# Kernel tuning notes

Measured on AMD Instinct MI355X. Metric: run time of the kernel, lower is better.

Reference implementation:

```python
import jax, jax.numpy as jnp
import numpy as np

EPS = 1e-5
R_MAX = 2.0
KPTS = 4

def silu(x):
    return x * jax.nn.sigmoid(x)

def conv1x1(x, w):  # w: (O, I)
    return jnp.einsum('oi,bihw->bohw', w, x)

def dwconv3(x, k):  # k: (C, 1, 3, 3), depthwise
    return jax.lax.conv_general_dilated(x, k, (1, 1), 'SAME',
        feature_group_count=x.shape[1], dimension_numbers=('NCHW', 'OIHW', 'NCHW'))

def conv3x3(x, k):  # k: (O, I, 3, 3)
    return jax.lax.conv_general_dilated(x, k, (1, 1), 'SAME',
        dimension_numbers=('NCHW', 'OIHW', 'NCHW'))

def bn_eval(x, g, b, m, v):
    scale = g / jnp.sqrt(v + EPS)
    return x * scale[None, :, None, None] + (b - m * scale)[None, :, None, None]

def ds_block(x, dw, pw, g, b, m, v):  # _DS: dwconv3 -> 1x1 -> BN -> SiLU
    return silu(bn_eval(conv1x1(dwconv3(x, dw), pw), g, b, m, v))

def offset_attn_head(q, w1, w2, b2):
    h = silu(conv3x3(q, w1))
    out = conv1x1(h, w2) + b2[None, :, None, None]
    B, _, H, W = out.shape
    off = out[:, :2 * KPTS].reshape(B, KPTS, 2, H, W)
    w = jax.nn.softmax(out[:, 2 * KPTS:].reshape(B, KPTS, H, W), axis=1)
    return off, w

def make_base_grid(Hf, Wf, Hc, Wc):
    yy, xx = jnp.meshgrid(jnp.arange(Hf, dtype=jnp.float32),
                          jnp.arange(Wf, dtype=jnp.float32), indexing='ij')
    xc = (xx + 0.5) * (Wc / Wf) - 0.5
    yc = (yy + 0.5) * (Hc / Hf) - 0.5
    gx = 2.0 * xc / max(Wc - 1, 1) - 1.0
    gy = 2.0 * yc / max(Hc - 1, 1) - 1.0
    return jnp.stack((gx, gy), axis=-1)  # (Hf, Wf, 2)

def avgpool(x, f):  # exact adaptive_avg_pool2d when H,W divisible by f
    B, C, H, W = x.shape
    return x.reshape(B, C, H // f, f, W // f, f).mean(axis=(3, 5))

def _gather(imgf, idx):  # imgf (C, HW), idx (K, Hf, Wf) -> (C, K, Hf, Wf)
    return imgf[:, idx]

def deform_sample(coarse, off, w, base, r_max=R_MAX):
    # bilinear grid_sample, padding_mode='border', align_corners=True
    B, C, Hc, Wc = coarse.shape
    K = off.shape[1]
    step_x = 2.0 / max(Wc - 1, 1)
    step_y = 2.0 / max(Hc - 1, 1)
    gx = base[..., 0][None, None] + jnp.tanh(off[:, :, 0]) * (r_max * step_x)  # (B,K,Hf,Wf)
    gy = base[..., 1][None, None] + jnp.tanh(off[:, :, 1]) * (r_max * step_y)
    ix = jnp.clip((gx + 1.0) * 0.5 * (Wc - 1), 0.0, Wc - 1)  # border padding = clamp
    iy = jnp.clip((gy + 1.0) * 0.5 * (Hc - 1), 0.0, Hc - 1)
    x0 = jnp.floor(ix); y0 = jnp.floor(iy)
    wx = (ix - x0)[:, None]  # (B,1,K,Hf,Wf)
    wy = (iy - y0)[:, None]
    x0i = x0.astype(jnp.int32); y0i = y0.astype(jnp.int32)
    x1i = jnp.minimum(x0i + 1, Wc - 1); y1i = jnp.minimum(y0i + 1, Hc - 1)
    imgf = coarse.reshape(B, C, Hc * Wc)
    g = jax.vmap(_gather)
    v00 = g(imgf, y0i * Wc + x0i)  # (B,C,K,Hf,Wf)
    v01 = g(imgf, y0i * Wc + x1i)
    v10 = g(imgf, y1i * Wc + x0i)
    v11 = g(imgf, y1i * Wc + x1i)
    samp = (v00 * (1 - wx) * (1 - wy) + v01 * wx * (1 - wy)
            + v10 * (1 - wx) * wy + v11 * wx * wy)
    return jnp.einsum('bkhw,bckhw->bchw', w, samp)

def csdm(x, ds0_dw, ds0_pw, ds0_g, ds0_b, ds0_m, ds0_v,
         ds1_dw, ds1_pw, ds1_g, ds1_b, ds1_m, ds1_v,
         ds2_dw, ds2_pw, ds2_g, ds2_b, ds2_m, ds2_v,
         qproj_w, h1_w1, h1_w2, h1_b2, h2_w1, h2_w2, h2_b2,
         r_w1, r_b1, r_w2, r_b2, final_w):
    B, C, H, W = x.shape
    s1 = avgpool(x, 2)
    s2 = avgpool(x, 4)
    z0 = ds_block(x,  ds0_dw, ds0_pw, ds0_g, ds0_b, ds0_m, ds0_v)
    z1 = ds_block(s1, ds1_dw, ds1_pw, ds1_g, ds1_b, ds1_m, ds1_v)
    z2 = ds_block(s2, ds2_dw, ds2_pw, ds2_g, ds2_b, ds2_m, ds2_v)
    q = conv1x1(z0, qproj_w)
    off1, w1 = offset_attn_head(q, h1_w1, h1_w2, h1_b2)
    off2, w2 = offset_attn_head(q, h2_w1, h2_w2, h2_b2)
    base1 = make_base_grid(H, W, z1.shape[2], z1.shape[3])
    base2 = make_base_grid(H, W, z2.shape[2], z2.shape[3])
    y1 = deform_sample(z1, off1, w1, base1)
    y2 = deform_sample(z2, off2, w2, base2)
    d0 = z0.mean(axis=(2, 3))
    d1 = y1.mean(axis=(2, 3))
    d2 = y2.mean(axis=(2, 3))
    hid = silu(jnp.concatenate([d0, d1, d2], axis=-1) @ r_w1 + r_b1)
    alpha = jax.nn.softmax(hid @ r_w2 + r_b2, axis=-1)  # (B, 3)
    a = alpha[:, :, None, None, None]
    out = a[:, 0] * z0 + a[:, 1] * y1 + a[:, 2] * y2
    return x + conv1x1(out, final_w)

def setup_inputs() -> dict:
    key = jax.random.key(0)
    B, C, H, W = 4, 32, 256, 256
    h, hr = 16, 32  # head hidden = max(4, int(C*0.5)); router hidden = max(16, C)
    ks = jax.random.split(key, 40)
    n = lambda i, shape, s=0.2: jax.random.normal(ks[i], shape, jnp.float32) * s
    inp = {'x': jax.random.normal(ks[0], (B, C, H, W), jnp.float32)}
    for j, p in enumerate(['ds0', 'ds1', 'ds2']):
        b = 1 + 6 * j
        inp[p + '_dw'] = n(b, (C, 1, 3, 3))
        inp[p + '_pw'] = n(b + 1, (C, C))
        inp[p + '_g'] = jnp.ones((C,), jnp.float32)
        inp[p + '_b'] = jnp.zeros((C,), jnp.float32)
        inp[p + '_m'] = n(b + 4, (C,), 0.1)
        inp[p + '_v'] = 1.0 + jax.random.uniform(ks[b + 5], (C,), jnp.float32) * 0.1
    inp['qproj_w'] = n(20, (C, C))
    inp['h1_w1'] = n(21, (h, C, 3, 3)); inp['h1_w2'] = n(22, (3 * KPTS, h)); inp['h1_b2'] = n(23, (3 * KPTS,), 0.1)
    inp['h2_w1'] = n(24, (h, C, 3, 3)); inp['h2_w2'] = n(25, (3 * KPTS, h)); inp['h2_b2'] = n(26, (3 * KPTS,), 0.1)
    inp['r_w1'] = n(27, (3 * C, hr)); inp['r_b1'] = n(28, (hr,), 0.1)
    inp['r_w2'] = n(29, (hr, 3)); inp['r_b2'] = n(30, (3,), 0.1)
    inp['final_w'] = n(31, (C, C))
    return inp

def reference(x, ds0_dw, ds0_pw, ds0_g, ds0_b, ds0_m, ds0_v,
              ds1_dw, ds1_pw, ds1_g, ds1_b, ds1_m, ds1_v,
              ds2_dw, ds2_pw, ds2_g, ds2_b, ds2_m, ds2_v,
              qproj_w, h1_w1, h1_w2, h1_b2, h2_w1, h2_w2, h2_b2,
              r_w1, r_b1, r_w2, r_b2, final_w):
    return csdm(x, ds0_dw, ds0_pw, ds0_g, ds0_b, ds0_m, ds0_v,
                ds1_dw, ds1_pw, ds1_g, ds1_b, ds1_m, ds1_v,
                ds2_dw, ds2_pw, ds2_g, ds2_b, ds2_m, ds2_v,
                qproj_w, h1_w1, h1_w2, h1_b2, h2_w1, h2_w2, h2_b2,
                r_w1, r_b1, r_w2, r_b2, final_w)
```

## Files before the change

kernel.cpp:

```cpp
#include <hip/hip_runtime.h>
#include <math.h>


constexpr int B = 4, C = 32, H = 256, W = 256;
constexpr int HW = H * W;
constexpr int H1 = 128, W1 = 128, HW1 = H1 * W1;
constexpr int H2 = 64,  W2 = 64,  HW2 = H2 * W2;
constexpr int CH = 16;
constexpr int CO = 12;
constexpr int TILE = 16;
constexpr int HALO = 18;
constexpr int TAREA = HALO * HALO;
constexpr int WP = 258;

typedef unsigned short ushort_t;
typedef __attribute__((ext_vector_type(8))) short bf16x8;
typedef __attribute__((ext_vector_type(4))) float f32x4;
typedef __attribute__((ext_vector_type(2))) float v2f;

static __device__ __forceinline__ float fast_rcp(float x) { return __builtin_amdgcn_rcpf(x); }
static __device__ __forceinline__ float silu_f(float x) { return x * fast_rcp(1.0f + __expf(-x)); }
static __device__ __forceinline__ v2f silu2(v2f x) {
    v2f r; r.x = silu_f(x.x); r.y = silu_f(x.y); return r;
}
static __device__ __forceinline__ float tanh_f(float x) {
    float xc = fminf(fmaxf(x, -15.0f), 15.0f);
    float e = __expf(2.0f * xc);
    return (e - 1.0f) * fast_rcp(e + 1.0f);
}
static __device__ __forceinline__ ushort_t f2b(float f) {
    unsigned u = __float_as_uint(f);
    return (ushort_t)((u + 0x7fffu + ((u >> 16) & 1u)) >> 16);
}
static __device__ __forceinline__ float bl(unsigned u) { return __uint_as_float(u << 16); }
static __device__ __forceinline__ float bh(unsigned u) { return __uint_as_float(u & 0xffff0000u); }
static __device__ __forceinline__ float wave_sum(float s) {
    s += __shfl_xor(s, 32, 64); s += __shfl_xor(s, 16, 64);
    s += __shfl_xor(s, 8, 64);  s += __shfl_xor(s, 4, 64);
    s += __shfl_xor(s, 2, 64);  s += __shfl_xor(s, 1, 64);
    return s;
}

static __device__ __forceinline__ float red8_ch(float v0, float v1, float v2, float v3,
                                                float v4, float v5, float v6, float v7,
                                                int lane) {
    bool q0 = (lane & 1) != 0, q1 = (lane & 2) != 0, q2 = (lane & 4) != 0;
    float a0 = (q0 ? v4 : v0) + __shfl_xor(q0 ? v0 : v4, 1, 64);
    float a1 = (q0 ? v5 : v1) + __shfl_xor(q0 ? v1 : v5, 1, 64);
    float a2 = (q0 ? v6 : v2) + __shfl_xor(q0 ? v2 : v6, 1, 64);
    float a3 = (q0 ? v7 : v3) + __shfl_xor(q0 ? v3 : v7, 1, 64);
    float c0 = (q1 ? a2 : a0) + __shfl_xor(q1 ? a0 : a2, 2, 64);
    float c1 = (q1 ? a3 : a1) + __shfl_xor(q1 ? a1 : a3, 2, 64);
    float e  = (q2 ? c1 : c0) + __shfl_xor(q2 ? c0 : c1, 4, 64);
    e += __shfl_xor(e, 8, 64);
    e += __shfl_xor(e, 16, 64);
    e += __shfl_xor(e, 32, 64);
    return e;
}

__global__ void pre_kernel(const float* __restrict__ x, float* __restrict__ s1,
                           ushort_t* __restrict__ qpad, float* __restrict__ dall,
                           const float* __restrict__ h1w1, const float* __restrict__ h2w1,
                           ushort_t* __restrict__ w1ra, ushort_t* __restrict__ w1rb) {
    int idx = blockIdx.x * blockDim.x + threadIdx.x;
    constexpr int NP = B * C * HW1;
    if (idx < NP) {
        int wo = idx % W1; int t = idx / W1;
        int ho = t % H1;   t /= H1;
        const float* src = x + ((size_t)t * H + (size_t)ho * 2) * W + (size_t)wo * 2;
        s1[idx] = (src[0] + src[1] + src[W] + src[W + 1]) * 0.25f;
        return;
    }
    int i = idx - NP;
    if (i < 4112) {
        int b = i / 1028, r = i % 1028;
        int y, xx;
        if (r < 258)      { y = 0;           xx = r; }
        else if (r < 516) { y = 257;         xx = r - 258; }
        else if (r < 772) { y = r - 516 + 1; xx = 0; }
        else              { y = r - 772 + 1; xx = 257; }
        uint4 z4 = {0, 0, 0, 0};
        uint4* p = (uint4*)(qpad + (((size_t)b * WP + y) * WP + xx) * 32);
        p[0] = z4; p[1] = z4; p[2] = z4; p[3] = z4;
        return;
    }
    i -= 4112;
    if (i < 512) { dall[i] = 0.0f; return; }
    i -= 512;
    if (i < 4608) {
        int o = i / 288, k = i - o * 288;
        int j = k >> 5, ci = k & 31;
        w1ra[i] = f2b(h1w1[(o * C + ci) * 9 + j]);
        return;
    }
    i -= 4608;
    if (i < 4608) {
        int o = i / 288, k = i - o * 288;
        int j = k >> 5, ci = k & 31;
        w1rb[i] = f2b(h2w1[(o * C + ci) * 9 + j]);
    }
}

__global__ void pool4_kernel(const float* __restrict__ s1, float* __restrict__ s2) {
    int idx = blockIdx.x * blockDim.x + threadIdx.x;
    if (idx >= B * C * HW2) return;
    int wo = idx % W2; int t = idx / W2;
    int ho = t % H2;   t /= H2;
    const float* src = s1 + ((size_t)t * H1 + (size_t)ho * 2) * W1 + (size_t)wo * 2;
    s2[idx] = (src[0] + src[1] + src[W1] + src[W1 + 1]) * 0.25f;
}

template<bool CHLAST>
__global__ __launch_bounds__(256, 4) void fused_ds_kernel(
        const float* __restrict__ in, const float* __restrict__ dw,
        const float* __restrict__ pw, const float* __restrict__ g,
        const float* __restrict__ bb, const float* __restrict__ m,
        const float* __restrict__ v, const float* __restrict__ qw,
        float* __restrict__ out, ushort_t* __restrict__ outcl,
        ushort_t* __restrict__ qout, float* __restrict__ dall,
        int Hs, int Ws, int tilesX) {
    __shared__ unsigned tileu[16 * TAREA];
    __shared__ v2f dwp[16 * 9];
    __shared__ v2f pwp[C * 16];
    __shared__ v2f qwp[CHLAST ? 1 : C * 16];
    __shared__ v2f scale2[16], shift2[16];
    __shared__ float zsum[CHLAST ? 1 : 4][CHLAST ? 1 : 32];
    int tid = threadIdx.x;
    int b = blockIdx.y;
    int HWs = Hs * Ws;
    int ox = (blockIdx.x % tilesX) * TILE;
    int oy = (blockIdx.x / tilesX) * TILE;

    for (int i = tid; i < 16 * 9; i += 256) {
        int c2 = i / 9, j = i - c2 * 9;
        dwp[i] = (v2f){dw[(2 * c2) * 9 + j], dw[(2 * c2 + 1) * 9 + j]};
    }
    for (int i = tid; i < C * 16; i += 256) {
        int ci = i >> 4, o2 = i & 15;
        pwp[i] = (v2f){pw[(2 * o2) * C + ci], pw[(2 * o2 + 1) * C + ci]};
        if (!CHLAST) qwp[i] = (v2f){qw[(2 * o2) * C + ci], qw[(2 * o2 + 1) * C + ci]};
    }
    if (tid < 16) {
        float s0 = g[2 * tid] * rsqrtf(v[2 * tid] + 1e-5f);
        float s1v = g[2 * tid + 1] * rsqrtf(v[2 * tid + 1] + 1e-5f);
        scale2[tid] = (v2f){s0, s1v};
        shift2[tid] = (v2f){bb[2 * tid] - m[2 * tid] * s0, bb[2 * tid + 1] - m[2 * tid + 1] * s1v};
    }
    const float* src = in + (size_t)b * C * HWs;
    for (int i = tid; i < 16 * TAREA; i += 256) {
        int c2 = i / TAREA, r = i - c2 * TAREA;
        int yy = r / HALO, xx = r - yy * HALO;
        int gy = oy - 1 + yy, gx = ox - 1 + xx;
        float v0 = 0.0f, v1 = 0.0f;
        if (gy >= 0 && gy < Hs && gx >= 0 && gx < Ws) {
            const float* sp = src + (size_t)(2 * c2) * HWs + gy * Ws + gx;
            v0 = sp[0]; v1 = sp[HWs];
        }
        tileu[i] = (unsigned)f2b(v0) | ((unsigned)f2b(v1) << 16);
    }
    __syncthreads();

    int tx = tid & 15, ty = tid >> 4;
    int off[9];
#pragma unroll
    for (int jy = 0; jy < 3; ++jy)
#pragma unroll
        for (int jx = 0; jx < 3; ++jx)
            off[jy * 3 + jx] = (ty + jy) * HALO + tx + jx;

    v2f t2[16];
#pragma unroll
    for (int c2 = 0; c2 < 16; ++c2) {
        v2f s = {0.0f, 0.0f};
        const unsigned* tp = tileu + c2 * TAREA;
#pragma unroll
        for (int j = 0; j < 9; ++j) {
            unsigned u = tp[off[j]];
            v2f val = {bl(u), bh(u)};
            s += dwp[c2 * 9 + j] * val;
        }
        t2[c2] = s;
    }

    v2f acc2[16];
#pragma unroll
    for (int o2 = 0; o2 < 16; ++o2) acc2[o2] = (v2f){0.0f, 0.0f};
#pragma unroll
    for (int i2 = 0; i2 < 16; ++i2) {
        float ta = t2[i2].x, tb = t2[i2].y;
        const v2f* r0 = pwp + (2 * i2) * 16;
        const v2f* r1 = r0 + 16;
#pragma unroll
        for (int o2 = 0; o2 < 16; ++o2)
            acc2[o2] += r0[o2] * ta + r1[o2] * tb;
    }
#pragma unroll
    for (int o2 = 0; o2 < 16; ++o2)
        acc2[o2] = silu2(acc2[o2] * scale2[o2] + shift2[o2]);

    int px = ox + tx, py = oy + ty;
    int p = py * Ws + px;
    if (CHLAST) {
        unsigned up[16];
#pragma unroll
        for (int j = 0; j < 16; ++j)
            up[j] = (unsigned)f2b(acc2[j].x) | ((unsigned)f2b(acc2[j].y) << 16);
        uint4* dst = (uint4*)(outcl + ((size_t)b * HWs + p) * C);
#pragma unroll
        for (int j = 0; j < 4; ++j)
            dst[j] = make_uint4(up[4 * j], up[4 * j + 1], up[4 * j + 2], up[4 * j + 3]);
    } else {
        float* dst = out + (size_t)b * C * HWs + p;
#pragma unroll
        for (int o2 = 0; o2 < 16; ++o2) {
            dst[(size_t)(2 * o2) * HWs] = acc2[o2].x;
            dst[(size_t)(2 * o2 + 1) * HWs] = acc2[o2].y;
        }
        v2f q2[16];
#pragma unroll
        for (int o2 = 0; o2 < 16; ++o2) q2[o2] = (v2f){0.0f, 0.0f};
#pragma unroll
        for (int i2 = 0; i2 < 16; ++i2) {
            float ta = acc2[i2].x, tb = acc2[i2].y;
            const v2f* r0 = qwp + (2 * i2) * 16;
            const v2f* r1 = r0 + 16;
#pragma unroll
            for (int o2 = 0; o2 < 16; ++o2)
                q2[o2] += r0[o2] * ta + r1[o2] * tb;
        }
        unsigned up[16];
#pragma unroll
        for (int j = 0; j < 16; ++j)
            up[j] = (unsigned)f2b(q2[j].x) | ((unsigned)f2b(q2[j].y) << 16);
        uint4* qd = (uint4*)(qout + (((size_t)b * WP + py + 1) * WP + px + 1) * 32);
#pragma unroll
        for (int j = 0; j < 4; ++j)
            qd[j] = make_uint4(up[4 * j], up[4 * j + 1], up[4 * j + 2], up[4 * j + 3]);
        int lane = tid & 63, wv = tid >> 6;
#pragma unroll
        for (int o2 = 0; o2 < 16; ++o2) {
            float sx = wave_sum(acc2[o2].x);
            float sy = wave_sum(acc2[o2].y);
            if (lane == 0) { zsum[wv][2 * o2] = sx; zsum[wv][2 * o2 + 1] = sy; }
        }
        __syncthreads();
        if (tid < 32)
            atomicAdd(&dall[b * 96 + tid],
                      (zsum[0][tid] + zsum[1][tid] + zsum[2][tid] + zsum[3][tid]) * (1.0f / HW));
    }
}

template<int HC, int WC>
static __device__ __forceinline__ void calc_off(const float* o12, int px, int py,
                                                int* zoff, float* wgt) {
    float mx = fmaxf(fmaxf(o12[8], o12[9]), fmaxf(o12[10], o12[11]));
    float e0 = __expf(o12[8] - mx), e1 = __expf(o12[9] - mx);
    float e2 = __expf(o12[10] - mx), e3 = __expf(o12[11] - mx);
    float inv = fast_rcp(e0 + e1 + e2 + e3);
    float wk4[4] = {e0 * inv, e1 * inv, e2 * inv, e3 * inv};
    float xc = (px + 0.5f) * ((float)WC / (float)W) - 0.5f;
    float yc = (py + 0.5f) * ((float)HC / (float)H) - 0.5f;
#pragma unroll
    for (int k = 0; k < 4; ++k) {
        float ix = fminf(fmaxf(xc + 2.0f * tanh_f(o12[2 * k]),     0.0f), (float)(WC - 1));
        float iy = fminf(fmaxf(yc + 2.0f * tanh_f(o12[2 * k + 1]), 0.0f), (float)(HC - 1));
        float x0f = floorf(ix), y0f = floorf(iy);
        int x0 = (int)x0f, y0 = (int)y0f;
        int x1 = min(x0 + 1, WC - 1), y1 = min(y0 + 1, HC - 1);
        float wx = ix - x0f, wy = iy - y0f;
        float wk = wk4[k];
        zoff[4 * k + 0] = (y0 * WC + x0) * C; wgt[4 * k + 0] = (1.0f - wx) * (1.0f - wy) * wk;
        zoff[4 * k + 1] = (y0 * WC + x1) * C; wgt[4 * k + 1] = wx * (1.0f - wy) * wk;
        zoff[4 * k + 2] = (y1 * WC + x0) * C; wgt[4 * k + 2] = (1.0f - wx) * wy * wk;
        zoff[4 * k + 3] = (y1 * WC + x1) * C; wgt[4 * k + 3] = wx * wy * wk;
    }
}

__global__ __launch_bounds__(256, 4) void head_deform_kernel(
        const ushort_t* __restrict__ qpad,
        const ushort_t* __restrict__ z1, const ushort_t* __restrict__ z2,
        const ushort_t* __restrict__ w1ra, const ushort_t* __restrict__ w1rb,
        const float* __restrict__ w2a, const float* __restrict__ b2a,
        const float* __restrict__ w2b, const float* __restrict__ b2b,
        float* __restrict__ y1, float* __restrict__ y2, float* __restrict__ dall) {
    __shared__ __align__(16) char smem[TAREA * C * 2];
    ushort_t* tile = (ushort_t*)smem;
    unsigned* hidw = (unsigned*)smem;
    float (*ysum)[32] = (float (*)[32])(smem + 9216);
    int tid = threadIdx.x, b = blockIdx.y, hsel = blockIdx.z;
    int ox = (blockIdx.x & 15) * TILE, oy = (blockIdx.x >> 4) * TILE;
    int lane = tid & 63, wv = tid >> 6;
    int n15 = lane & 15, quad = lane >> 4;
    int tx = tid & 15, ty = tid >> 4;

    {
        const ushort_t* base = qpad + ((size_t)b * WP + oy) * WP * 32;
        uint4* tl = (uint4*)tile;
        for (int i = tid; i < 1296; i += 256) {
            int yy = i / 72, r = i - yy * 72;
            tl[i] = *(const uint4*)(base + ((size_t)yy * WP + ox) * 32 + r * 8);
        }
    }
    __syncthreads();

    const ushort_t* w1r = hsel ? w1rb : w1ra;
    bf16x8 af[9];
#pragma unroll
    for (int j = 0; j < 9; ++j)
        af[j] = *(const bf16x8*)(w1r + n15 * 288 + j * 32 + quad * 8);
    unsigned pk[8];
#pragma unroll
    for (int g = 0; g < 4; ++g) {
        int yrow = wv * 4 + g;
        f32x4 acc = {0.0f, 0.0f, 0.0f, 0.0f};
#pragma unroll
        for (int jy = 0; jy < 3; ++jy)
#pragma unroll
            for (int jx = 0; jx < 3; ++jx) {
                const bf16x8* bp = (const bf16x8*)(tile +
                    ((yrow + jy) * HALO + n15 + jx) * 32 + quad * 8);
                acc = __builtin_amdgcn_mfma_f32_16x16x32_bf16(
                    af[jy * 3 + jx], *bp, acc, 0, 0, 0);
            }
        pk[2 * g]     = (unsigned)f2b(acc[0]) | ((unsigned)f2b(acc[1]) << 16);
        pk[2 * g + 1] = (unsigned)f2b(acc[2]) | ((unsigned)f2b(acc[3]) << 16);
    }
    __syncthreads();
#pragma unroll
    for (int g = 0; g < 4; ++g) {
        int pxl = (wv * 4 + g) * 16 + n15;
        hidw[pxl * 9 + quad * 2]     = pk[2 * g];
        hidw[pxl * 9 + quad * 2 + 1] = pk[2 * g + 1];
    }
    float hid[CH];
#pragma unroll
    for (int j = 0; j < 8; ++j) {
        unsigned u = hidw[tid * 9 + j];
        hid[2 * j]     = silu_f(bl(u));
        hid[2 * j + 1] = silu_f(bh(u));
    }

    const float* w2 = hsel ? w2b : w2a;
    const float* bs = hsel ? b2b : b2a;
    float o12[CO];
#pragma unroll
    for (int j = 0; j < CO; ++j) {
        float a = bs[j];
#pragma unroll
        for (int i = 0; i < CH; ++i) a += w2[j * CH + i] * hid[i];
        o12[j] = a;
    }
    int px = ox + tx, py = oy + ty;
    int off[16]; float wg[16];
    if (hsel == 0) calc_off<H1, W1>(o12, px, py, off, wg);
    else           calc_off<H2, W2>(o12, px, py, off, wg);

    const ushort_t* zb = hsel ? z2 + (size_t)b * HW2 * C : z1 + (size_t)b * HW1 * C;
    int p = py * W + px;
    float* d = (hsel ? y2 : y1) + (size_t)b * C * HW + p;

#pragma unroll
    for (int c8 = 0; c8 < 4; ++c8) {
        uint4 vv[16];
#pragma unroll
        for (int j = 0; j < 16; ++j)
            vv[j] = *(const uint4*)(zb + off[j] + c8 * 8);
        f32x4 lo = {0.0f, 0.0f, 0.0f, 0.0f};
        f32x4 hi = {0.0f, 0.0f, 0.0f, 0.0f};
#pragma unroll
        for (int j = 0; j < 16; ++j) {
            float wj = wg[j];
            lo[0] += wj * bl(vv[j].x); lo[1] += wj * bh(vv[j].x);
            lo[2] += wj * bl(vv[j].y); lo[3] += wj * bh(vv[j].y);
            hi[0] += wj * bl(vv[j].z); hi[1] += wj * bh(vv[j].z);
            hi[2] += wj * bl(vv[j].w); hi[3] += wj * bh(vv[j].w);
        }
#pragma unroll
        for (int k = 0; k < 4; ++k) {
            d[(size_t)(c8 * 8 + k) * HW]     = lo[k];
            d[(size_t)(c8 * 8 + 4 + k) * HW] = hi[k];
        }
        float s = red8_ch(lo[0], lo[1], lo[2], lo[3], hi[0], hi[1], hi[2], hi[3], lane);
        if (lane < 8)
            ysum[wv][c8 * 8 + ((lane & 1) * 4 + (lane & 2) + ((lane >> 2) & 1))] = s;
    }
    __syncthreads();
    if (tid < 32) {
        float s = ysum[0][tid] + ysum[1][tid] + ysum[2][tid] + ysum[3][tid];
        atomicAdd(&dall[b * 96 + 32 + hsel * 32 + tid], s * (1.0f / HW));
    }
}

__global__ void gate_kernel(const float* __restrict__ dall,
                            const float* __restrict__ w1, const float* __restrict__ b1,
                            const float* __restrict__ w2, const float* __restrict__ b2,
                            float* __restrict__ alpha) {
    __shared__ float hid[B][32];
    int tid = threadIdx.x;
    int b = tid >> 5, j = tid & 31;
    float a = b1[j];
    for (int k = 0; k < 96; ++k) a += dall[b * 96 + k] * w1[k * 32 + j];
    hid[b][j] = silu_f(a);
    __syncthreads();
    if (j == 0) {
        float lg[3];
#pragma unroll
        for (int t = 0; t < 3; ++t) {
            float acc = b2[t];
            for (int jj = 0; jj < 32; ++jj) acc += hid[b][jj] * w2[jj * 3 + t];
            lg[t] = acc;
        }
        float mx = fmaxf(lg[0], fmaxf(lg[1], lg[2]));
        float e0 = __expf(lg[0] - mx), e1 = __expf(lg[1] - mx), e2 = __expf(lg[2] - mx);
        float inv = fast_rcp(e0 + e1 + e2);
        alpha[b * 3 + 0] = e0 * inv;
        alpha[b * 3 + 1] = e1 * inv;
        alpha[b * 3 + 2] = e2 * inv;
    }
}

__global__ __launch_bounds__(256, 4) void final_kernel(
        const float* __restrict__ x,
        const float* __restrict__ z0, const float* __restrict__ y1,
        const float* __restrict__ y2, const float* __restrict__ alpha,
        const float* __restrict__ fw, float* __restrict__ out) {
    __shared__ float ws[C * C];
    for (int i = threadIdx.x; i < C * C; i += blockDim.x) ws[i] = fw[i];
    __syncthreads();
    int idx = blockIdx.x * blockDim.x + threadIdx.x;
    constexpr int HP = HW / 2;
    if (idx >= B * HP) return;
    int b = idx / HP, p = (idx - b * HP) * 2;
    float a0 = alpha[b * 3], a1 = alpha[b * 3 + 1], a2 = alpha[b * 3 + 2];
    size_t base = (size_t)b * C * HW + p;
    v2f mix[C];
#pragma unroll
    for (int i = 0; i < C; ++i) {
        size_t e = base + (size_t)i * HW;
        v2f za = *(const v2f*)(z0 + e);
        v2f ya = *(const v2f*)(y1 + e);
        v2f yb = *(const v2f*)(y2 + e);
        mix[i] = a0 * za + a1 * ya + a2 * yb;
    }
#pragma unroll 4
    for (int o = 0; o < C; ++o) {
        v2f acc = {0.0f, 0.0f};
#pragma unroll
        for (int i = 0; i < C; ++i) acc += ws[o * C + i] * mix[i];
        size_t e = base + (size_t)o * HW;
        v2f xr = *(const v2f*)(x + e);
        *(v2f*)(out + e) = acc + xr;
    }
}

extern "C" void kernel_launch(void* const* d_in, const int* in_sizes, int n_in,
                              void* d_out, int out_size, void* d_ws, size_t ws_size,
                              hipStream_t stream) {
    const float* x       = (const float*)d_in[0];
    const float* ds_dw[3] = {(const float*)d_in[1],  (const float*)d_in[7],  (const float*)d_in[13]};
    const float* ds_pw[3] = {(const float*)d_in[2],  (const float*)d_in[8],  (const float*)d_in[14]};
    const float* ds_g[3]  = {(const float*)d_in[3],  (const float*)d_in[9],  (const float*)d_in[15]};
    const float* ds_b[3]  = {(const float*)d_in[4],  (const float*)d_in[10], (const float*)d_in[16]};
    const float* ds_m[3]  = {(const float*)d_in[5],  (const float*)d_in[11], (const float*)d_in[17]};
    const float* ds_v[3]  = {(const float*)d_in[6],  (const float*)d_in[12], (const float*)d_in[18]};
    const float* qproj_w = (const float*)d_in[19];
    const float* h1_w1   = (const float*)d_in[20];
    const float* h1_w2   = (const float*)d_in[21];
    const float* h1_b2   = (const float*)d_in[22];
    const float* h2_w1   = (const float*)d_in[23];
    const float* h2_w2   = (const float*)d_in[24];
    const float* h2_b2   = (const float*)d_in[25];
    const float* r_w1    = (const float*)d_in[26];
    const float* r_b1    = (const float*)d_in[27];
    const float* r_w2    = (const float*)d_in[28];
    const float* r_b2    = (const float*)d_in[29];
    const float* final_w = (const float*)d_in[30];
    float* out = (float*)d_out;

    constexpr size_t N0 = (size_t)B * C * HW;
    constexpr size_t N1 = (size_t)B * C * HW1;
    constexpr size_t N2 = (size_t)B * C * HW2;
    constexpr size_t NQ = ((size_t)B * WP * WP * 32 + 1) / 2;

    float* w = (float*)d_ws;
    float* z0   = w; w += N0;
    float* y1   = w; w += N0;
    float* y2   = w; w += N0;
    ushort_t* z1cl = (ushort_t*)w; w += N1 / 2;
    ushort_t* z2cl = (ushort_t*)w; w += N2 / 2;
    float* s1   = w; w += N1;
    float* s2   = w; w += N2;
    ushort_t* qpad = (ushort_t*)w; w += NQ;
    ushort_t* w1ra = (ushort_t*)w; w += 2304;
    ushort_t* w1rb = (ushort_t*)w; w += 2304;
    float* dall  = w; w += 512;
    float* alpha = w; w += 16;
    (void)ws_size; (void)in_sizes; (void)n_in; (void)out_size;

    const int T = 256;
    auto g = [](size_t n, int t) { return (int)((n + t - 1) / t); };

    pre_kernel<<<g(N1 + 4112 + 512 + 9216, T), T, 0, stream>>>(
        x, s1, qpad, dall, h1_w1, h2_w1, w1ra, w1rb);
    pool4_kernel<<<g(N2, T), T, 0, stream>>>(s1, s2);

    fused_ds_kernel<false><<<dim3((H / TILE) * (W / TILE), B), T, 0, stream>>>(
        x, ds_dw[0], ds_pw[0], ds_g[0], ds_b[0], ds_m[0], ds_v[0], qproj_w,
        z0, nullptr, qpad, dall, H, W, W / TILE);
    fused_ds_kernel<true><<<dim3((H1 / TILE) * (W1 / TILE), B), T, 0, stream>>>(
        s1, ds_dw[1], ds_pw[1], ds_g[1], ds_b[1], ds_m[1], ds_v[1], nullptr,
        nullptr, z1cl, nullptr, nullptr, H1, W1, W1 / TILE);
    fused_ds_kernel<true><<<dim3((H2 / TILE) * (W2 / TILE), B), T, 0, stream>>>(
        s2, ds_dw[2], ds_pw[2], ds_g[2], ds_b[2], ds_m[2], ds_v[2], nullptr,
        nullptr, z2cl, nullptr, nullptr, H2, W2, W2 / TILE);

    head_deform_kernel<<<dim3((H / TILE) * (W / TILE), B, 2), T, 0, stream>>>(
        qpad, z1cl, z2cl, w1ra, w1rb, h1_w2, h1_b2, h2_w2, h2_b2, y1, y2, dall);

    gate_kernel<<<1, 128, 0, stream>>>(dall, r_w1, r_b1, r_w2, r_b2, alpha);

    final_kernel<<<g((size_t)B * HW / 2, T), T, 0, stream>>>(x, z0, y1, y2, alpha, final_w, out);
}
```

Baseline: 327.3 us.

## Merge pyramid pooling and three DS levels into fewer launches

Computes the 4x4 pooled input directly from x inside pre_kernel, which removes the separate pool4 launch and its dependency on s1. The three per-level depthwise-separable kernel launches are merged into one grid whose blocks pick their level from blockIdx, so the small coarse levels run concurrently with the fine level instead of serializing. The channel-sum reduction also switches from 32 full wave_sum butterflies to the packed red8_ch reduction, cutting shuffle count. In exchange the merged kernel loses template specialization, adding runtime branches and possibly more register pressure for the coarse-level blocks.

```diff
diff --git a/kernel.cpp b/kernel.cpp
--- a/kernel.cpp
+++ b/kernel.cpp
@@ -34,12 +34,6 @@
 }
 static __device__ __forceinline__ float bl(unsigned u) { return __uint_as_float(u << 16); }
 static __device__ __forceinline__ float bh(unsigned u) { return __uint_as_float(u & 0xffff0000u); }
-static __device__ __forceinline__ float wave_sum(float s) {
-    s += __shfl_xor(s, 32, 64); s += __shfl_xor(s, 16, 64);
-    s += __shfl_xor(s, 8, 64);  s += __shfl_xor(s, 4, 64);
-    s += __shfl_xor(s, 2, 64);  s += __shfl_xor(s, 1, 64);
-    return s;
-}
 
 static __device__ __forceinline__ float red8_ch(float v0, float v1, float v2, float v3,
                                                 float v4, float v5, float v6, float v7,
@@ -59,11 +53,13 @@
 }
 
 __global__ void pre_kernel(const float* __restrict__ x, float* __restrict__ s1,
+                           float* __restrict__ s2,
                            ushort_t* __restrict__ qpad, float* __restrict__ dall,
                            const float* __restrict__ h1w1, const float* __restrict__ h2w1,
                            ushort_t* __restrict__ w1ra, ushort_t* __restrict__ w1rb) {
     int idx = blockIdx.x * blockDim.x + threadIdx.x;
     constexpr int NP = B * C * HW1;
+    constexpr int NP2 = B * C * HW2;
     if (idx < NP) {
         int wo = idx % W1; int t = idx / W1;
         int ho = t % H1;   t /= H1;
@@ -72,6 +68,20 @@
         return;
     }
     int i = idx - NP;
+    if (i < NP2) {
+        int wo = i % W2; int t = i / W2;
+        int ho = t % H2;   t /= H2;
+        const float* src = x + ((size_t)t * H + (size_t)ho * 4) * W + (size_t)wo * 4;
+        float s = 0.0f;
+#pragma unroll
+        for (int r = 0; r < 4; ++r) {
+            const float* rp = src + (size_t)r * W;
+            s += (rp[0] + rp[1]) + (rp[2] + rp[3]);
+        }
+        s2[i] = s * 0.0625f;
+        return;
+    }
+    i -= NP2;
     if (i < 4112) {
         int b = i / 1028, r = i % 1028;
         int y, xx;
@@ -101,52 +111,55 @@
     }
 }
 
-__global__ void pool4_kernel(const float* __restrict__ s1, float* __restrict__ s2) {
-    int idx = blockIdx.x * blockDim.x + threadIdx.x;
-    if (idx >= B * C * HW2) return;
-    int wo = idx % W2; int t = idx / W2;
-    int ho = t % H2;   t /= H2;
-    const float* src = s1 + ((size_t)t * H1 + (size_t)ho * 2) * W1 + (size_t)wo * 2;
-    s2[idx] = (src[0] + src[1] + src[W1] + src[W1 + 1]) * 0.25f;
-}
-
-template<bool CHLAST>
-__global__ __launch_bounds__(256, 4) void fused_ds_kernel(
-        const float* __restrict__ in, const float* __restrict__ dw,
-        const float* __restrict__ pw, const float* __restrict__ g,
-        const float* __restrict__ bb, const float* __restrict__ m,
-        const float* __restrict__ v, const float* __restrict__ qw,
-        float* __restrict__ out, ushort_t* __restrict__ outcl,
-        ushort_t* __restrict__ qout, float* __restrict__ dall,
-        int Hs, int Ws, int tilesX) {
+struct DsParams {
+    const float* in; const float* dw; const float* pw;
+    const float* g;  const float* b;  const float* m; const float* v;
+};
+
+__global__ __launch_bounds__(256, 4) void fused_ds_all_kernel(
+        DsParams P0, DsParams P1, DsParams P2, const float* __restrict__ qw,
+        float* __restrict__ z0out, ushort_t* __restrict__ z1cl,
+        ushort_t* __restrict__ z2cl, ushort_t* __restrict__ qout,
+        float* __restrict__ dall) {
     __shared__ unsigned tileu[16 * TAREA];
     __shared__ v2f dwp[16 * 9];
     __shared__ v2f pwp[C * 16];
-    __shared__ v2f qwp[CHLAST ? 1 : C * 16];
+    __shared__ v2f qwp[C * 16];
     __shared__ v2f scale2[16], shift2[16];
-    __shared__ float zsum[CHLAST ? 1 : 4][CHLAST ? 1 : 32];
+    __shared__ float zsum[4][32];
+
+    int bx = blockIdx.x;
+    int level = (bx < 1024) ? 0 : (bx < 1280 ? 1 : 2);
+    int rel = bx - ((level == 0) ? 0 : (level == 1 ? 1024 : 1280));
+    int Hs = (level == 0) ? H : (level == 1 ? H1 : H2);
+    int Ws = Hs;
+    int tilesX = Ws / TILE;
+    int tilesT = tilesX * (Hs / TILE);
+    int b = rel / tilesT;
+    int tile = rel - b * tilesT;
+    int ox = (tile % tilesX) * TILE;
+    int oy = (tile / tilesX) * TILE;
+    DsParams P = (level == 0) ? P0 : (level == 1 ? P1 : P2);
+    int HWs = Hs * Ws;
     int tid = threadIdx.x;
-    int b = blockIdx.y;
-    int HWs = Hs * Ws;
-    int ox = (blockIdx.x % tilesX) * TILE;
-    int oy = (blockIdx.x / tilesX) * TILE;
 
     for (int i = tid; i < 16 * 9; i += 256) {
         int c2 = i / 9, j = i - c2 * 9;
-        dwp[i] = (v2f){dw[(2 * c2) * 9 + j], dw[(2 * c2 + 1) * 9 + j]};
+        dwp[i] = (v2f){P.dw[(2 * c2) * 9 + j], P.dw[(2 * c2 + 1) * 9 + j]};
     }
     for (int i = tid; i < C * 16; i += 256) {
         int ci = i >> 4, o2 = i & 15;
-        pwp[i] = (v2f){pw[(2 * o2) * C + ci], pw[(2 * o2 + 1) * C + ci]};
-        if (!CHLAST) qwp[i] = (v2f){qw[(2 * o2) * C + ci], qw[(2 * o2 + 1) * C + ci]};
+        pwp[i] = (v2f){P.pw[(2 * o2) * C + ci], P.pw[(2 * o2 + 1) * C + ci]};
+        if (level == 0) qwp[i] = (v2f){qw[(2 * o2) * C + ci], qw[(2 * o2 + 1) * C + ci]};
     }
     if (tid < 16) {
-        float s0 = g[2 * tid] * rsqrtf(v[2 * tid] + 1e-5f);
-        float s1v = g[2 * tid + 1] * rsqrtf(v[2 * tid + 1] + 1e-5f);
+        float s0 = P.g[2 * tid] * rsqrtf(P.v[2 * tid] + 1e-5f);
+        float s1v = P.g[2 * tid + 1] * rsqrtf(P.v[2 * tid + 1] + 1e-5f);
         scale2[tid] = (v2f){s0, s1v};
-        shift2[tid] = (v2f){bb[2 * tid] - m[2 * tid] * s0, bb[2 * tid + 1] - m[2 * tid + 1] * s1v};
-    }
-    const float* src = in + (size_t)b * C * HWs;
+        shift2[tid] = (v2f){P.b[2 * tid] - P.m[2 * tid] * s0,
+                            P.b[2 * tid + 1] - P.m[2 * tid + 1] * s1v};
+    }
+    const float* src = P.in + (size_t)b * C * HWs;
     for (int i = tid; i < 16 * TAREA; i += 256) {
         int c2 = i / TAREA, r = i - c2 * TAREA;
         int yy = r / HALO, xx = r - yy * HALO;
@@ -200,7 +213,8 @@
 
     int px = ox + tx, py = oy + ty;
     int p = py * Ws + px;
-    if (CHLAST) {
+    if (level > 0) {
+        ushort_t* outcl = (level == 1) ? z1cl : z2cl;
         unsigned up[16];
 #pragma unroll
         for (int j = 0; j < 16; ++j)
@@ -210,7 +224,7 @@
         for (int j = 0; j < 4; ++j)
             dst[j] = make_uint4(up[4 * j], up[4 * j + 1], up[4 * j + 2], up[4 * j + 3]);
     } else {
-        float* dst = out + (size_t)b * C * HWs + p;
+        float* dst = z0out + (size_t)b * C * HWs + p;
 #pragma unroll
         for (int o2 = 0; o2 < 16; ++o2) {
             dst[(size_t)(2 * o2) * HWs] = acc2[o2].x;
@@ -238,10 +252,13 @@
             qd[j] = make_uint4(up[4 * j], up[4 * j + 1], up[4 * j + 2], up[4 * j + 3]);
         int lane = tid & 63, wv = tid >> 6;
 #pragma unroll
-        for (int o2 = 0; o2 < 16; ++o2) {
-            float sx = wave_sum(acc2[o2].x);
-            float sy = wave_sum(acc2[o2].y);
-            if (lane == 0) { zsum[wv][2 * o2] = sx; zsum[wv][2 * o2 + 1] = sy; }
+        for (int gq = 0; gq < 4; ++gq) {
+            float s = red8_ch(acc2[4 * gq].x,     acc2[4 * gq].y,
+                              acc2[4 * gq + 1].x, acc2[4 * gq + 1].y,
+                              acc2[4 * gq + 2].x, acc2[4 * gq + 2].y,
+                              acc2[4 * gq + 3].x, acc2[4 * gq + 3].y, lane);
+            if (lane < 8)
+                zsum[wv][8 * gq + ((lane & 1) * 4 + (lane & 2) + ((lane >> 2) & 1))] = s;
         }
         __syncthreads();
         if (tid < 32)
@@ -500,19 +517,14 @@
     const int T = 256;
     auto g = [](size_t n, int t) { return (int)((n + t - 1) / t); };
 
-    pre_kernel<<<g(N1 + 4112 + 512 + 9216, T), T, 0, stream>>>(
-        x, s1, qpad, dall, h1_w1, h2_w1, w1ra, w1rb);
-    pool4_kernel<<<g(N2, T), T, 0, stream>>>(s1, s2);
-
-    fused_ds_kernel<false><<<dim3((H / TILE) * (W / TILE), B), T, 0, stream>>>(
-        x, ds_dw[0], ds_pw[0], ds_g[0], ds_b[0], ds_m[0], ds_v[0], qproj_w,
-        z0, nullptr, qpad, dall, H, W, W / TILE);
-    fused_ds_kernel<true><<<dim3((H1 / TILE) * (W1 / TILE), B), T, 0, stream>>>(
-        s1, ds_dw[1], ds_pw[1], ds_g[1], ds_b[1], ds_m[1], ds_v[1], nullptr,
-        nullptr, z1cl, nullptr, nullptr, H1, W1, W1 / TILE);
-    fused_ds_kernel<true><<<dim3((H2 / TILE) * (W2 / TILE), B), T, 0, stream>>>(
-        s2, ds_dw[2], ds_pw[2], ds_g[2], ds_b[2], ds_m[2], ds_v[2], nullptr,
-        nullptr, z2cl, nullptr, nullptr, H2, W2, W2 / TILE);
+    pre_kernel<<<g(N1 + N2 + 4112 + 512 + 9216, T), T, 0, stream>>>(
+        x, s1, s2, qpad, dall, h1_w1, h2_w1, w1ra, w1rb);
+
+    DsParams p0 = {x,  ds_dw[0], ds_pw[0], ds_g[0], ds_b[0], ds_m[0], ds_v[0]};
+    DsParams p1 = {s1, ds_dw[1], ds_pw[1], ds_g[1], ds_b[1], ds_m[1], ds_v[1]};
+    DsParams p2 = {s2, ds_dw[2], ds_pw[2], ds_g[2], ds_b[2], ds_m[2], ds_v[2]};
+    fused_ds_all_kernel<<<1344, T, 0, stream>>>(
+        p0, p1, p2, qproj_w, z0, z1cl, z2cl, qpad, dall);
 
     head_deform_kernel<<<dim3((H / TILE) * (W / TILE), B, 2), T, 0, stream>>>(
         qpad, z1cl, z2cl, w1ra, w1rb, h1_w2, h1_b2, h2_w2, h2_b2, y1, y2, dall);
```

Result: faster. 299.2 us (-8.6%).
